# Kernel optimization log

Measured on AMD Instinct MI355X. Metric: run time of the kernel, lower is better.

## Reference

```python
import jax, jax.numpy as jnp
import numpy as np

N_SAMPLES = 8_388_608   # total packed samples (~64 per ray on average)
N_RAYS = 131_072
DT_SCALE = 0.005        # keep per-ray optical depth ~O(1); also tempers global-cumsum fp32 error


def setup_inputs() -> dict:
    key = jax.random.key(0)
    k1, k2, k3, k4, k5 = jax.random.split(key, 5)
    rgb_samples = jax.random.uniform(k1, (N_SAMPLES, 3), dtype=jnp.float32)
    radiance_samples = jax.random.uniform(k2, (N_SAMPLES, 1), dtype=jnp.float32)  # density sigma >= 0
    samples_z = jax.random.uniform(k3, (N_SAMPLES,), dtype=jnp.float32)           # t values in [0,1)
    samples_dt = jax.random.uniform(k4, (N_SAMPLES,), dtype=jnp.float32) * DT_SCALE
    # sorted segment ids == contiguous packed per-ray sample ranges (ragged)
    ray_id = jnp.sort(jax.random.randint(k5, (N_SAMPLES,), 0, N_RAYS, dtype=jnp.int64))
    ray_t_exit = jnp.full((N_RAYS, 1), 2.0, dtype=jnp.float32)  # exit t beyond all z -> positive last dt
    return {
        "rgb_samples": rgb_samples,
        "radiance_samples": radiance_samples,
        "samples_z": samples_z,
        "samples_dt": samples_dt,
        "ray_id": ray_id,
        "ray_t_exit": ray_t_exit,
        "use_ray_t_exit": 1,
    }


def reference(rgb_samples, radiance_samples, samples_z, samples_dt, ray_id, ray_t_exit, use_ray_t_exit):
    N = rgb_samples.shape[0]
    sigma = radiance_samples[:, 0]
    idx = jnp.arange(N)

    # dt of the last sample of each ray is (t_exit - z_last) when use_ray_t_exit
    if use_ray_t_exit:
        last_idx = jax.ops.segment_max(idx, ray_id, num_segments=N_RAYS)
        is_last = idx == last_idx[ray_id]
        dt = jnp.where(is_last, ray_t_exit[ray_id, 0] - samples_z, samples_dt)
    else:
        dt = samples_dt

    sigdt = sigma * dt                      # optical depth per sample
    c = jnp.cumsum(sigdt)                   # global inclusive cumsum
    c_excl = c - sigdt                      # global exclusive cumsum
    # exclusive cumsum restarted per ray: subtract value at each segment's first sample
    # (c_excl is non-decreasing since sigdt >= 0, so segment_min == first element)
    seg_start = jax.ops.segment_min(c_excl, ray_id, num_segments=N_RAYS)
    T = jnp.exp(-(c_excl - seg_start[ray_id]))          # transmittance before each sample
    alpha = 1.0 - jnp.exp(-sigdt)
    w = alpha * T                                        # per-sample compositing weight

    pred_rgb = jax.ops.segment_sum(w[:, None] * rgb_samples, ray_id, num_segments=N_RAYS)   # [R,3]
    pred_depth = jax.ops.segment_sum(w * samples_z, ray_id, num_segments=N_RAYS)[:, None]   # [R,1]
    bg_transmittance = jnp.exp(-jax.ops.segment_sum(sigdt, ray_id, num_segments=N_RAYS))[:, None]  # [R,1]
    weight_per_sample = w[:, None]                                                           # [N,1]
    return pred_rgb, pred_depth, bg_transmittance, weight_per_sample
```

## Files before the change

kernel.cpp:

```cpp
#include <hip/hip_runtime.h>


#define RPW 4

typedef float __attribute__((ext_vector_type(2))) f32x2;
typedef float __attribute__((ext_vector_type(4))) f32x4;

__device__ __forceinline__ f32x2 async_load2(const float* p) {
    f32x2 r;
    asm volatile("global_load_dwordx2 %0, %1, off" : "=v"(r) : "v"(p));
    return r;
}
__device__ __forceinline__ f32x4 async_load4(const float* p) {
    f32x4 r;
    asm volatile("global_load_dwordx4 %0, %1, off" : "=v"(r) : "v"(p));
    return r;
}

template <int CTRL, int ROW_MASK>
__device__ __forceinline__ float dpp_add(float x) {
    int t = __builtin_amdgcn_update_dpp(0, __float_as_int(x), CTRL, ROW_MASK, 0xf, true);
    return x + __int_as_float(t);
}

__device__ __forceinline__ float wave_incl_scan(float x) {
    x = dpp_add<0x111, 0xf>(x);
    x = dpp_add<0x112, 0xf>(x);
    x = dpp_add<0x114, 0xf>(x);
    x = dpp_add<0x118, 0xf>(x);
    x = dpp_add<0x142, 0xa>(x);
    x = dpp_add<0x143, 0xc>(x);
    return x;
}

__device__ __forceinline__ float readlane_f32(float x, int lane) {
    return __int_as_float(__builtin_amdgcn_readlane(__float_as_int(x), lane));
}

__global__ void compute_starts_kernel(const int* __restrict__ ray_id,
                                      int n_samples, int n_rays,
                                      int* __restrict__ starts) {
    const int t = blockIdx.x * blockDim.x + threadIdx.x;
    const int stride = gridDim.x * blockDim.x;
    if (t == 0) {
        const int first = ray_id[0];
        for (int r = 0; r <= first; ++r) starts[r] = 0;
        const int last = ray_id[n_samples - 1];
        for (int r = last + 1; r <= n_rays; ++r) starts[r] = n_samples;
    }
    for (int g = t; g * 4 < n_samples; g += stride) {
        const int i4 = g * 4;
        const int4 v = *reinterpret_cast<const int4*>(ray_id + i4);
        const int prev = (i4 == 0) ? v.x : ray_id[i4 - 1];
        const int vals[5] = {prev, v.x, v.y, v.z, v.w};
        #pragma unroll
        for (int j = 0; j < 4; ++j) {
            const int p = vals[j], c = vals[j + 1];
            if (c != p) {
                for (int r = p + 1; r <= c; ++r) starts[r] = i4 + j;
            }
        }
    }
}

__device__ __forceinline__ void process_pass128_rare(
    const float* __restrict__ sigma_in, const float* __restrict__ z_in,
    const float* __restrict__ dt_in, const float* __restrict__ rgb,
    int base, int s1, int lane, int use_exit, float texit, int n_samples,
    float& csum, float& carry,
    float& aR, float& aG, float& aB, float& aD,
    float* __restrict__ out_w)
{
    const int i0 = base + 2 * lane, i1 = i0 + 1;
    const int il = min(i0, n_samples - 2);
    float sgx = sigma_in[il],     sgy = sigma_in[il + 1];
    float zvx = z_in[il],         zvy = z_in[il + 1];
    float dtx = dt_in[il],        dty = dt_in[il + 1];
    float c0 = rgb[3 * (size_t)il + 0], c1 = rgb[3 * (size_t)il + 1], c2 = rgb[3 * (size_t)il + 2];
    float c3 = rgb[3 * (size_t)il + 3], c4 = rgb[3 * (size_t)il + 4], c5 = rgb[3 * (size_t)il + 5];
    if (i0 > n_samples - 2) {
        sgx = sgy; zvx = zvy; dtx = dty; c0 = c3; c1 = c4; c2 = c5;
    }
    if (use_exit && i0 == s1 - 1) dtx = texit - zvx;
    if (use_exit && i1 == s1 - 1) dty = texit - zvy;
    const float e0 = (i0 < s1) ? sgx * dtx : 0.f;
    const float e1 = (i1 < s1) ? sgy * dty : 0.f;
    const float t1 = csum + wave_incl_scan(e0 + e1);
    const float v0 = __expf(-(t1 - e1));
    const float v1 = __expf(-t1);
    const int vpi = __builtin_amdgcn_update_dpp(__float_as_int(carry), __float_as_int(v1),
                                                0x138 , 0xf, 0xf, false);
    const float w0 = __int_as_float(vpi) - v0;
    const float w1 = v0 - v1;
    if (i0 < s1) out_w[i0] = w0;
    if (i1 < s1) out_w[i1] = w1;
    aR += w0 * c0 + w1 * c3;
    aG += w0 * c1 + w1 * c4;
    aB += w0 * c2 + w1 * c5;
    aD += w0 * zvx + w1 * zvy;
    csum  = readlane_f32(t1, 63);
    carry = readlane_f32(v1, 63);
}

__global__ __launch_bounds__(256) void render_kernel(
    const float* __restrict__ rgb,
    const float* __restrict__ sigma_in,
    const float* __restrict__ z_in,
    const float* __restrict__ dt_in,
    const float* __restrict__ t_exit,
    const int*  __restrict__ use_exit_p,
    const int*  __restrict__ starts,
    float* __restrict__ out_rgb,
    float* __restrict__ out_depth,
    float* __restrict__ out_bg,
    float* __restrict__ out_w,
    int n_rays, int n_samples)
{
    const int wave = threadIdx.x >> 6;
    const int lane = threadIdx.x & 63;
    const int wid  = blockIdx.x * (blockDim.x >> 6) + wave;
    const int ray0 = wid * RPW;

    const int use_exit = *use_exit_p;

    int s[RPW + 1];
    #pragma unroll
    for (int k = 0; k <= RPW; ++k) {
        s[k] = __builtin_amdgcn_readfirstlane(starts[min(ray0 + k, n_rays)]);
    }
    float tex[RPW];
    #pragma unroll
    for (int k = 0; k < RPW; ++k) {
        tex[k] = readlane_f32(t_exit[min(ray0 + k, n_rays - 1)], 0);
    }

    f32x2 sg[RPW], zv[RPW], dtv[RPW], c45[RPW];
    f32x4 c03[RPW];
    #pragma unroll
    for (int k = 0; k < RPW; ++k) {
        const int i0 = s[k] + 2 * lane;
        const int il = min(i0, n_samples - 2);
        sg[k]  = async_load2(sigma_in + il);
        zv[k]  = async_load2(z_in + il);
        dtv[k] = async_load2(dt_in + il);
        c03[k] = async_load4(rgb + 3 * (size_t)il);
        c45[k] = async_load2(rgb + 3 * (size_t)il + 4);
    }
    asm volatile("s_waitcnt vmcnt(0)" ::: "memory");
    __builtin_amdgcn_sched_barrier(0);

    float accR[RPW], accG[RPW], accB[RPW], accD[RPW];
    float w0v[RPW], w1v[RPW], t1v[RPW], v1v[RPW];
    #pragma unroll
    for (int k = 0; k < RPW; ++k) {
        const int s1 = s[k + 1];
        const int i0 = s[k] + 2 * lane;
        const int i1 = i0 + 1;
        const bool clamped = i0 > n_samples - 2;
        const float sgx = clamped ? sg[k].y : sg[k].x;
        const float sgy = sg[k].y;
        const float zvx = clamped ? zv[k].y : zv[k].x;
        const float zvy = zv[k].y;
        float dt0 = clamped ? dtv[k].y : dtv[k].x;
        float dt1 = dtv[k].y;
        const float cc0 = clamped ? c03[k].w : c03[k].x;
        const float cc1 = clamped ? c45[k].x : c03[k].y;
        const float cc2 = clamped ? c45[k].y : c03[k].z;
        const float cc3 = c03[k].w;
        const float cc4 = c45[k].x;
        const float cc5 = c45[k].y;
        if (use_exit && i0 == s1 - 1) dt0 = tex[k] - zvx;
        if (use_exit && i1 == s1 - 1) dt1 = tex[k] - zvy;
        const float e0 = (i0 < s1) ? sgx * dt0 : 0.f;
        const float e1 = (i1 < s1) ? sgy * dt1 : 0.f;
        const float t1 = wave_incl_scan(e0 + e1);
        const float v0 = __expf(-(t1 - e1));
        const float v1 = __expf(-t1);
        const int vpi = __builtin_amdgcn_update_dpp(0x3f800000 , __float_as_int(v1),
                                                    0x138 , 0xf, 0xf, false);
        const float vp = __int_as_float(vpi);
        const float w0 = vp - v0;
        const float w1 = v0 - v1;
        w0v[k] = w0;  w1v[k] = w1;
        accR[k] = w0 * cc0 + w1 * cc3;
        accG[k] = w0 * cc1 + w1 * cc4;
        accB[k] = w0 * cc2 + w1 * cc5;
        accD[k] = w0 * zvx + w1 * zvy;
        t1v[k] = t1;  v1v[k] = v1;
    }

    bool anylong = false;
    #pragma unroll
    for (int k = 0; k < RPW; ++k) anylong |= (s[k] + 128 < s[k + 1]);
    if (anylong) {
        #pragma unroll
        for (int k = 0; k < RPW; ++k) {
            float csum  = readlane_f32(t1v[k], 63);
            float carry = readlane_f32(v1v[k], 63);
            for (int base = s[k] + 128; base < s[k + 1]; base += 128) {
                process_pass128_rare(sigma_in, z_in, dt_in, rgb,
                                     base, s[k + 1], lane, use_exit, tex[k], n_samples,
                                     csum, carry, accR[k], accG[k], accB[k], accD[k], out_w);
            }
            v1v[k] = carry;
        }
    }

    #pragma unroll
    for (int k = 0; k < RPW; ++k) {
        const int s1 = s[k + 1];
        const int i0 = s[k] + 2 * lane;
        if (i0 < s1)     out_w[i0]     = w0v[k];
        if (i0 + 1 < s1) out_w[i0 + 1] = w1v[k];
    }

    #pragma unroll
    for (int k = 0; k < RPW; ++k) {
        const float r = wave_incl_scan(accR[k]);
        const float g = wave_incl_scan(accG[k]);
        const float b = wave_incl_scan(accB[k]);
        const float d = wave_incl_scan(accD[k]);
        const int ray = ray0 + k;
        if (lane == 63 && ray < n_rays) {
            out_rgb[3 * ray + 0] = r;
            out_rgb[3 * ray + 1] = g;
            out_rgb[3 * ray + 2] = b;
            out_depth[ray] = d;
            out_bg[ray]    = v1v[k];
        }
    }
}

extern "C" void kernel_launch(void* const* d_in, const int* in_sizes, int n_in,
                              void* d_out, int out_size, void* d_ws, size_t ws_size,
                              hipStream_t stream) {
    const float* rgb     = (const float*)d_in[0];
    const float* sigma   = (const float*)d_in[1];
    const float* z       = (const float*)d_in[2];
    const float* dt      = (const float*)d_in[3];
    const int*   ray_id  = (const int*)d_in[4];
    const float* t_exit  = (const float*)d_in[5];
    const int*   use_ex  = (const int*)d_in[6];

    const int n_samples = in_sizes[2];
    const int n_rays    = in_sizes[5];

    int* starts = (int*)d_ws;

    float* out      = (float*)d_out;
    float* out_rgb  = out;
    float* out_dep  = out + (size_t)3 * n_rays;
    float* out_bg   = out + (size_t)4 * n_rays;
    float* out_w    = out + (size_t)5 * n_rays;

    compute_starts_kernel<<<2048, 256, 0, stream>>>(ray_id, n_samples, n_rays, starts);

    const int waves_per_block = 4;
    const int rays_per_block  = waves_per_block * RPW;
    const int blocks = (n_rays + rays_per_block - 1) / rays_per_block;
    render_kernel<<<blocks, 256, 0, stream>>>(rgb, sigma, z, dt, t_exit, use_ex,
                                              starts, out_rgb, out_dep, out_bg,
                                              out_w, n_rays, n_samples);
}
```

Baseline: 55.52 us.

## Make render waves process many rays with double-buffered load pipelining

Each wave now handles 32 rays in pairs instead of 4 rays. It keeps two two-ray buffers of sample loads in flight and uses partial vmcnt waits so the loads for the next pair overlap the scan and compositing of the current pair. Ray starts and exit times are fetched once per wave with one vector load and read per lane, and launch bounds request higher occupancy. In exchange the grid becomes much smaller, with fewer resident waves per CU, so memory-level parallelism may drop on a bandwidth-bound kernel.

```diff
diff --git a/kernel.cpp b/kernel.cpp
--- a/kernel.cpp
+++ b/kernel.cpp
@@ -1,21 +1,13 @@
 #include <hip/hip_runtime.h>
 
 
-#define RPW 4
+#define NGROUP 16
+#define RPW 2
 
 typedef float __attribute__((ext_vector_type(2))) f32x2;
 typedef float __attribute__((ext_vector_type(4))) f32x4;
 
-__device__ __forceinline__ f32x2 async_load2(const float* p) {
-    f32x2 r;
-    asm volatile("global_load_dwordx2 %0, %1, off" : "=v"(r) : "v"(p));
-    return r;
-}
-__device__ __forceinline__ f32x4 async_load4(const float* p) {
-    f32x4 r;
-    asm volatile("global_load_dwordx4 %0, %1, off" : "=v"(r) : "v"(p));
-    return r;
-}
+struct Pay { f32x2 sg, zv, dt, c45; f32x4 c03; };
 
 template <int CTRL, int ROW_MASK>
 __device__ __forceinline__ float dpp_add(float x) {
@@ -61,6 +53,24 @@
             }
         }
     }
+}
+
+__device__ __forceinline__ void issue_ray(Pay& p,
+                                          const float* __restrict__ sigma_in,
+                                          const float* __restrict__ z_in,
+                                          const float* __restrict__ dt_in,
+                                          const float* __restrict__ rgb,
+                                          int s0, int lane, int imax2) {
+    const int il = min(s0 + 2 * lane, imax2);
+    const float* a = sigma_in + il;
+    const float* b = z_in + il;
+    const float* c = dt_in + il;
+    const float* d = rgb + 3 * (size_t)il;
+    asm volatile("global_load_dwordx2 %0, %1, off" : "=v"(p.sg)  : "v"(a));
+    asm volatile("global_load_dwordx2 %0, %1, off" : "=v"(p.zv)  : "v"(b));
+    asm volatile("global_load_dwordx2 %0, %1, off" : "=v"(p.dt)  : "v"(c));
+    asm volatile("global_load_dwordx4 %0, %1, off" : "=v"(p.c03) : "v"(d));
+    asm volatile("global_load_dwordx2 %0, %1, off" : "=v"(p.c45) : "v"(d + 4));
 }
 
 __device__ __forceinline__ void process_pass128_rare(
@@ -78,9 +88,7 @@
     float dtx = dt_in[il],        dty = dt_in[il + 1];
     float c0 = rgb[3 * (size_t)il + 0], c1 = rgb[3 * (size_t)il + 1], c2 = rgb[3 * (size_t)il + 2];
     float c3 = rgb[3 * (size_t)il + 3], c4 = rgb[3 * (size_t)il + 4], c5 = rgb[3 * (size_t)il + 5];
-    if (i0 > n_samples - 2) {
-        sgx = sgy; zvx = zvy; dtx = dty; c0 = c3; c1 = c4; c2 = c5;
-    }
+    if (i0 > n_samples - 2) { sgx = sgy; zvx = zvy; dtx = dty; c0 = c3; c1 = c4; c2 = c5; }
     if (use_exit && i0 == s1 - 1) dtx = texit - zvx;
     if (use_exit && i1 == s1 - 1) dty = texit - zvy;
     const float e0 = (i0 < s1) ? sgx * dtx : 0.f;
@@ -102,7 +110,70 @@
     carry = readlane_f32(v1, 63);
 }
 
-__global__ __launch_bounds__(256) void render_kernel(
+__device__ __forceinline__ void compute_ray(
+    const Pay& p, int ray, int s0, int s1, int lane, int use_exit, float texit,
+    int n_samples, int n_rays,
+    const float* __restrict__ sigma_in, const float* __restrict__ z_in,
+    const float* __restrict__ dt_in, const float* __restrict__ rgb,
+    float* __restrict__ out_rgb, float* __restrict__ out_depth,
+    float* __restrict__ out_bg, float* __restrict__ out_w)
+{
+    const int i0 = s0 + 2 * lane, i1 = i0 + 1;
+    const bool clamped = i0 > n_samples - 2;
+    const float sgx = clamped ? p.sg.y : p.sg.x;
+    const float sgy = p.sg.y;
+    const float zvx = clamped ? p.zv.y : p.zv.x;
+    const float zvy = p.zv.y;
+    float dt0 = clamped ? p.dt.y : p.dt.x;
+    float dt1 = p.dt.y;
+    const float cc0 = clamped ? p.c03.w : p.c03.x;
+    const float cc1 = clamped ? p.c45.x : p.c03.y;
+    const float cc2 = clamped ? p.c45.y : p.c03.z;
+    const float cc3 = p.c03.w, cc4 = p.c45.x, cc5 = p.c45.y;
+    if (use_exit && i0 == s1 - 1) dt0 = texit - zvx;
+    if (use_exit && i1 == s1 - 1) dt1 = texit - zvy;
+    const float e0 = (i0 < s1) ? sgx * dt0 : 0.f;
+    const float e1 = (i1 < s1) ? sgy * dt1 : 0.f;
+    const float t1 = wave_incl_scan(e0 + e1);
+    const float v0 = __expf(-(t1 - e1));
+    const float v1 = __expf(-t1);
+    const int vpi = __builtin_amdgcn_update_dpp(0x3f800000 , __float_as_int(v1),
+                                                0x138 , 0xf, 0xf, false);
+    const float w0 = __int_as_float(vpi) - v0;
+    const float w1 = v0 - v1;
+    float accR = w0 * cc0 + w1 * cc3;
+    float accG = w0 * cc1 + w1 * cc4;
+    float accB = w0 * cc2 + w1 * cc5;
+    float accD = w0 * zvx + w1 * zvy;
+    if (i0 < s1) out_w[i0] = w0;
+    if (i1 < s1) out_w[i1] = w1;
+    float bg = readlane_f32(v1, 63);
+
+    if (__builtin_expect(s0 + 128 < s1, 0)) {
+        float csum  = readlane_f32(t1, 63);
+        float carry = bg;
+        for (int base = s0 + 128; base < s1; base += 128) {
+            process_pass128_rare(sigma_in, z_in, dt_in, rgb, base, s1, lane,
+                                 use_exit, texit, n_samples,
+                                 csum, carry, accR, accG, accB, accD, out_w);
+        }
+        bg = carry;
+    }
+
+    const float r = wave_incl_scan(accR);
+    const float g = wave_incl_scan(accG);
+    const float b = wave_incl_scan(accB);
+    const float d = wave_incl_scan(accD);
+    if (lane == 63 && ray < n_rays) {
+        out_rgb[3 * ray + 0] = r;
+        out_rgb[3 * ray + 1] = g;
+        out_rgb[3 * ray + 2] = b;
+        out_depth[ray] = d;
+        out_bg[ray]    = bg;
+    }
+}
+
+__global__ __launch_bounds__(256, 4) void render_kernel(
     const float* __restrict__ rgb,
     const float* __restrict__ sigma_in,
     const float* __restrict__ z_in,
@@ -118,116 +189,92 @@
 {
     const int wave = threadIdx.x >> 6;
     const int lane = threadIdx.x & 63;
-    const int wid  = blockIdx.x * (blockDim.x >> 6) + wave;
-    const int ray0 = wid * RPW;
-
-    const int use_exit = *use_exit_p;
-
-    int s[RPW + 1];
-    #pragma unroll
-    for (int k = 0; k <= RPW; ++k) {
-        s[k] = __builtin_amdgcn_readfirstlane(starts[min(ray0 + k, n_rays)]);
-    }
-    float tex[RPW];
-    #pragma unroll
-    for (int k = 0; k < RPW; ++k) {
-        tex[k] = readlane_f32(t_exit[min(ray0 + k, n_rays - 1)], 0);
-    }
-
-    f32x2 sg[RPW], zv[RPW], dtv[RPW], c45[RPW];
-    f32x4 c03[RPW];
-    #pragma unroll
-    for (int k = 0; k < RPW; ++k) {
-        const int i0 = s[k] + 2 * lane;
-        const int il = min(i0, n_samples - 2);
-        sg[k]  = async_load2(sigma_in + il);
-        zv[k]  = async_load2(z_in + il);
-        dtv[k] = async_load2(dt_in + il);
-        c03[k] = async_load4(rgb + 3 * (size_t)il);
-        c45[k] = async_load2(rgb + 3 * (size_t)il + 4);
+    const int wid  = blockIdx.x * 4 + wave;
+    const int r0   = wid * (NGROUP * RPW);
+    const int use_exit = __builtin_amdgcn_readfirstlane(*use_exit_p);
+    const int imax2 = n_samples - 2;
+
+    int sv; float tv;
+    {
+        const int* sp = starts + min(r0 + lane, n_rays);
+        asm volatile("global_load_dword %0, %1, off" : "=v"(sv) : "v"(sp));
+        const float* tp = t_exit + min(r0 + lane, n_rays - 1);
+        asm volatile("global_load_dword %0, %1, off" : "=v"(tv) : "v"(tp));
     }
     asm volatile("s_waitcnt vmcnt(0)" ::: "memory");
     __builtin_amdgcn_sched_barrier(0);
 
-    float accR[RPW], accG[RPW], accB[RPW], accD[RPW];
-    float w0v[RPW], w1v[RPW], t1v[RPW], v1v[RPW];
-    #pragma unroll
-    for (int k = 0; k < RPW; ++k) {
-        const int s1 = s[k + 1];
-        const int i0 = s[k] + 2 * lane;
-        const int i1 = i0 + 1;
-        const bool clamped = i0 > n_samples - 2;
-        const float sgx = clamped ? sg[k].y : sg[k].x;
-        const float sgy = sg[k].y;
-        const float zvx = clamped ? zv[k].y : zv[k].x;
-        const float zvy = zv[k].y;
-        float dt0 = clamped ? dtv[k].y : dtv[k].x;
-        float dt1 = dtv[k].y;
-        const float cc0 = clamped ? c03[k].w : c03[k].x;
-        const float cc1 = clamped ? c45[k].x : c03[k].y;
-        const float cc2 = clamped ? c45[k].y : c03[k].z;
-        const float cc3 = c03[k].w;
-        const float cc4 = c45[k].x;
-        const float cc5 = c45[k].y;
-        if (use_exit && i0 == s1 - 1) dt0 = tex[k] - zvx;
-        if (use_exit && i1 == s1 - 1) dt1 = tex[k] - zvy;
-        const float e0 = (i0 < s1) ? sgx * dt0 : 0.f;
-        const float e1 = (i1 < s1) ? sgy * dt1 : 0.f;
-        const float t1 = wave_incl_scan(e0 + e1);
-        const float v0 = __expf(-(t1 - e1));
-        const float v1 = __expf(-t1);
-        const int vpi = __builtin_amdgcn_update_dpp(0x3f800000 , __float_as_int(v1),
-                                                    0x138 , 0xf, 0xf, false);
-        const float vp = __int_as_float(vpi);
-        const float w0 = vp - v0;
-        const float w1 = v0 - v1;
-        w0v[k] = w0;  w1v[k] = w1;
-        accR[k] = w0 * cc0 + w1 * cc3;
-        accG[k] = w0 * cc1 + w1 * cc4;
-        accB[k] = w0 * cc2 + w1 * cc5;
-        accD[k] = w0 * zvx + w1 * zvy;
-        t1v[k] = t1;  v1v[k] = v1;
-    }
-
-    bool anylong = false;
-    #pragma unroll
-    for (int k = 0; k < RPW; ++k) anylong |= (s[k] + 128 < s[k + 1]);
-    if (anylong) {
-        #pragma unroll
-        for (int k = 0; k < RPW; ++k) {
-            float csum  = readlane_f32(t1v[k], 63);
-            float carry = readlane_f32(v1v[k], 63);
-            for (int base = s[k] + 128; base < s[k + 1]; base += 128) {
-                process_pass128_rare(sigma_in, z_in, dt_in, rgb,
-                                     base, s[k + 1], lane, use_exit, tex[k], n_samples,
-                                     csum, carry, accR[k], accG[k], accB[k], accD[k], out_w);
-            }
-            v1v[k] = carry;
+    Pay A0, A1, B0, B1;
+    issue_ray(A0, sigma_in, z_in, dt_in, rgb, __builtin_amdgcn_readlane(sv, 0), lane, imax2);
+    issue_ray(A1, sigma_in, z_in, dt_in, rgb, __builtin_amdgcn_readlane(sv, 1), lane, imax2);
+    issue_ray(B0, sigma_in, z_in, dt_in, rgb, __builtin_amdgcn_readlane(sv, 2), lane, imax2);
+    issue_ray(B1, sigma_in, z_in, dt_in, rgb, __builtin_amdgcn_readlane(sv, 3), lane, imax2);
+
+    int g = 0;
+    #pragma unroll 1
+    for (int it = 0; it < (NGROUP - 2) / 2; ++it) {
+        {
+            const int j = 2 * g;
+            asm volatile("s_waitcnt vmcnt(10)" ::: "memory");
+            __builtin_amdgcn_sched_barrier(0);
+            const int s0a = __builtin_amdgcn_readlane(sv, j);
+            const int s1a = __builtin_amdgcn_readlane(sv, j + 1);
+            const int s2a = __builtin_amdgcn_readlane(sv, j + 2);
+            const float tx0 = readlane_f32(tv, j);
+            const float tx1 = readlane_f32(tv, j + 1);
+            compute_ray(A0, r0 + j,     s0a, s1a, lane, use_exit, tx0, n_samples, n_rays,
+                        sigma_in, z_in, dt_in, rgb, out_rgb, out_depth, out_bg, out_w);
+            compute_ray(A1, r0 + j + 1, s1a, s2a, lane, use_exit, tx1, n_samples, n_rays,
+                        sigma_in, z_in, dt_in, rgb, out_rgb, out_depth, out_bg, out_w);
+            issue_ray(A0, sigma_in, z_in, dt_in, rgb,
+                      __builtin_amdgcn_readlane(sv, j + 4), lane, imax2);
+            issue_ray(A1, sigma_in, z_in, dt_in, rgb,
+                      __builtin_amdgcn_readlane(sv, j + 5), lane, imax2);
         }
-    }
-
-    #pragma unroll
-    for (int k = 0; k < RPW; ++k) {
-        const int s1 = s[k + 1];
-        const int i0 = s[k] + 2 * lane;
-        if (i0 < s1)     out_w[i0]     = w0v[k];
-        if (i0 + 1 < s1) out_w[i0 + 1] = w1v[k];
-    }
-
-    #pragma unroll
-    for (int k = 0; k < RPW; ++k) {
-        const float r = wave_incl_scan(accR[k]);
-        const float g = wave_incl_scan(accG[k]);
-        const float b = wave_incl_scan(accB[k]);
-        const float d = wave_incl_scan(accD[k]);
-        const int ray = ray0 + k;
-        if (lane == 63 && ray < n_rays) {
-            out_rgb[3 * ray + 0] = r;
-            out_rgb[3 * ray + 1] = g;
-            out_rgb[3 * ray + 2] = b;
-            out_depth[ray] = d;
-            out_bg[ray]    = v1v[k];
+        {
+            const int j = 2 * g + 2;
+            asm volatile("s_waitcnt vmcnt(10)" ::: "memory");
+            __builtin_amdgcn_sched_barrier(0);
+            const int s0b = __builtin_amdgcn_readlane(sv, j);
+            const int s1b = __builtin_amdgcn_readlane(sv, j + 1);
+            const int s2b = __builtin_amdgcn_readlane(sv, j + 2);
+            const float tx0 = readlane_f32(tv, j);
+            const float tx1 = readlane_f32(tv, j + 1);
+            compute_ray(B0, r0 + j,     s0b, s1b, lane, use_exit, tx0, n_samples, n_rays,
+                        sigma_in, z_in, dt_in, rgb, out_rgb, out_depth, out_bg, out_w);
+            compute_ray(B1, r0 + j + 1, s1b, s2b, lane, use_exit, tx1, n_samples, n_rays,
+                        sigma_in, z_in, dt_in, rgb, out_rgb, out_depth, out_bg, out_w);
+            issue_ray(B0, sigma_in, z_in, dt_in, rgb,
+                      __builtin_amdgcn_readlane(sv, j + 4), lane, imax2);
+            issue_ray(B1, sigma_in, z_in, dt_in, rgb,
+                      __builtin_amdgcn_readlane(sv, j + 5), lane, imax2);
         }
+        g += 2;
+    }
+
+    {
+        const int j = 2 * (NGROUP - 2);
+        asm volatile("s_waitcnt vmcnt(10)" ::: "memory");
+        __builtin_amdgcn_sched_barrier(0);
+        const int s0a = __builtin_amdgcn_readlane(sv, j);
+        const int s1a = __builtin_amdgcn_readlane(sv, j + 1);
+        const int s2a = __builtin_amdgcn_readlane(sv, j + 2);
+        compute_ray(A0, r0 + j,     s0a, s1a, lane, use_exit, readlane_f32(tv, j), n_samples, n_rays,
+                    sigma_in, z_in, dt_in, rgb, out_rgb, out_depth, out_bg, out_w);
+        compute_ray(A1, r0 + j + 1, s1a, s2a, lane, use_exit, readlane_f32(tv, j + 1), n_samples, n_rays,
+                    sigma_in, z_in, dt_in, rgb, out_rgb, out_depth, out_bg, out_w);
+    }
+    {
+        const int j = 2 * (NGROUP - 1);
+        asm volatile("s_waitcnt vmcnt(0)" ::: "memory");
+        __builtin_amdgcn_sched_barrier(0);
+        const int s0b = __builtin_amdgcn_readlane(sv, j);
+        const int s1b = __builtin_amdgcn_readlane(sv, j + 1);
+        const int s2b = __builtin_amdgcn_readlane(sv, j + 2);
+        compute_ray(B0, r0 + j,     s0b, s1b, lane, use_exit, readlane_f32(tv, j), n_samples, n_rays,
+                    sigma_in, z_in, dt_in, rgb, out_rgb, out_depth, out_bg, out_w);
+        compute_ray(B1, r0 + j + 1, s1b, s2b, lane, use_exit, readlane_f32(tv, j + 1), n_samples, n_rays,
+                    sigma_in, z_in, dt_in, rgb, out_rgb, out_depth, out_bg, out_w);
     }
 }
 
@@ -255,8 +302,7 @@
 
     compute_starts_kernel<<<2048, 256, 0, stream>>>(ray_id, n_samples, n_rays, starts);
 
-    const int waves_per_block = 4;
-    const int rays_per_block  = waves_per_block * RPW;
+    const int rays_per_block = 4 * NGROUP * RPW;
     const int blocks = (n_rays + rays_per_block - 1) / rays_per_block;
     render_kernel<<<blocks, 256, 0, stream>>>(rgb, sigma, z, dt, t_exit, use_ex,
                                               starts, out_rgb, out_dep, out_bg,
```

Result: slower. 62.48 us (+12.5%).
